# Optimization experiments

Measured on AMD Instinct MI355X. Metric: run time of the kernel, lower is better.

## Reference

```python
import jax, jax.numpy as jnp
import numpy as np

N_HEAD = 16
W = 128  # one-sided window = attention_window // 2


def setup_inputs() -> dict:
    key = jax.random.key(0)
    ks = jax.random.split(key, 6)
    B, S, D = 4, 1536, 1024
    init = lambda k: jax.random.normal(k, (D, D), jnp.float32) * 0.02
    return {
        "x": jax.random.normal(ks[0], (B, S, D), jnp.float32),
        "Wq": init(ks[1]), "bq": jnp.zeros((D,), jnp.float32),
        "Wk": init(ks[2]),
        "Wv": init(ks[3]), "bv": jnp.zeros((D,), jnp.float32),
        "Wo": init(ks[4]), "bo": jnp.zeros((D,), jnp.float32),
    }


def _local_attention(q, k, v, w):
    """Sliding-window attention. q,k,v: [B,H,S,Dh]; q,k pre-scaled.
    Returns context [B,H,S,Dh] and banded logits qk [B,S,H,2w+1] (fp32)."""
    B, H, S, Dh = q.shape
    C = S // w  # number of w-sized query chunks
    pad = [(0, 0), (0, 0), (w, w), (0, 0)]
    kp = jnp.pad(k, pad)
    vp = jnp.pad(v, pad)
    # key/value chunks: chunk c sees padded positions [c*w, c*w + 3w)
    idx = jnp.arange(C)[:, None] * w + jnp.arange(3 * w)[None, :]  # [C,3w]
    kc = kp[:, :, idx]                      # [B,H,C,3w,Dh]
    vc = vp[:, :, idx]                      # [B,H,C,3w,Dh]
    qc = q.reshape(B, H, C, w, Dh)          # [B,H,C,w,Dh]
    scores = jnp.einsum('bhcxd,bhcyd->bhcxy', qc, kc)  # [B,H,C,w,3w]
    # extract diagonal band: query x attends to chunk-local keys y = x .. x+2w
    xi = jnp.arange(w)[:, None]             # [w,1]
    jj = jnp.arange(2 * w + 1)[None, :]     # [1,2w+1]
    y = xi + jj                             # [w,2w+1], values in [0,3w)
    band = jnp.take_along_axis(scores, y[None, None, None], axis=-1)  # [B,H,C,w,2w+1]
    # mask positions whose absolute key index falls outside [0,S)
    key_pos = jnp.arange(C)[:, None, None] * w + xi[None] + jj[None] - w  # [C,w,2w+1]
    valid = (key_pos >= 0) & (key_pos < S)
    band = jnp.where(valid[None, None], band, -jnp.inf)
    prob = jax.nn.softmax(band.astype(jnp.float32), axis=-1).astype(q.dtype)
    # scatter band probs back to chunk layout, then contract with value chunks
    scat = jnp.zeros_like(scores).at[..., xi, y].set(prob)  # [B,H,C,w,3w]
    ctx = jnp.einsum('bhcxy,bhcyd->bhcxd', scat, vc).reshape(B, H, S, Dh)
    qk = band.astype(jnp.float32).reshape(B, H, S, 2 * w + 1).transpose(0, 2, 1, 3)
    return ctx, qk


def reference(x, Wq, bq, Wk, Wv, bv, Wo, bo):
    B, S, D = x.shape
    H, Dh = N_HEAD, D // N_HEAD
    scale = Dh ** (-0.25)
    q = ((x @ Wq.T + bq).reshape(B, S, H, Dh).transpose(0, 2, 1, 3)) * scale
    k = ((x @ Wk.T).reshape(B, S, H, Dh).transpose(0, 2, 1, 3)) * scale
    v = (x @ Wv.T + bv).reshape(B, S, H, Dh).transpose(0, 2, 1, 3)
    ctx, qk = _local_attention(q, k, v, W)
    wv = ctx.transpose(0, 2, 1, 3).reshape(B, S, D)
    out = wv @ Wo.T + bo
    return out, qk
```

## Files before the change

### kernel.cpp

```cpp
#include <hip/hip_runtime.h>

#define S_LEN  1536
#define NH     16
#define DHEAD  64
#define WIN    128
#define BAND   257
#define DMODEL 1024
#define BATCH  4
#define MROWS  (BATCH * S_LEN)

#define SQ    32
#define SWIN  (SQ + 2*WIN)
#define WKEYS 320
#define PST   296

#define NEG_BIG (-3.0e38f)

typedef __attribute__((ext_vector_type(8))) short frag_ab;
typedef __attribute__((ext_vector_type(4))) float frag_cd;
typedef __attribute__((ext_vector_type(8))) unsigned short ushort8v;

__device__ __forceinline__ unsigned short f2bf(float f) {
  unsigned u = __float_as_uint(f);
  u += 0x7FFFu + ((u >> 16) & 1u);
  return (unsigned short)(u >> 16);
}
__device__ __forceinline__ float bf2f(unsigned short h) {
  return __uint_as_float(((unsigned)h) << 16);
}

__device__ __forceinline__ void gload16(const unsigned short* g, unsigned short* l) {
  __builtin_amdgcn_global_load_lds(
      (const __attribute__((address_space(1))) unsigned int*)g,
      (__attribute__((address_space(3))) unsigned int*)l, 16, 0, 0);
}

__global__ __launch_bounds__(256)
void convert_hilo(const float* __restrict__ src, unsigned short* __restrict__ hi,
                  unsigned short* __restrict__ lo, int n4)
{
  const int i = blockIdx.x * 256 + threadIdx.x;
  if (i >= n4) return;
  const float4 v = reinterpret_cast<const float4*>(src)[i];
  unsigned short h0 = f2bf(v.x), h1 = f2bf(v.y), h2 = f2bf(v.z), h3 = f2bf(v.w);
  unsigned short l0 = f2bf(v.x - bf2f(h0)), l1 = f2bf(v.y - bf2f(h1));
  unsigned short l2 = f2bf(v.z - bf2f(h2)), l3 = f2bf(v.w - bf2f(h3));
  uint2 hp, lp;
  hp.x = (unsigned)h0 | ((unsigned)h1 << 16); hp.y = (unsigned)h2 | ((unsigned)h3 << 16);
  lp.x = (unsigned)l0 | ((unsigned)l1 << 16); lp.y = (unsigned)l2 | ((unsigned)l3 << 16);
  reinterpret_cast<uint2*>(hi)[i] = hp;
  reinterpret_cast<uint2*>(lo)[i] = lp;
}

__global__ __launch_bounds__(256)
void copy_f4(const float4* __restrict__ src, float4* __restrict__ dst, int n4)
{
  const int i = blockIdx.x * 256 + threadIdx.x;
  if (i < n4) dst[i] = src[i];
}

__global__ __launch_bounds__(256)
void mfma_gemm_bt(const unsigned short* __restrict__ Ah_g,
                  const unsigned short* __restrict__ Al_g,
                  const unsigned short* __restrict__ Bh_g,
                  const unsigned short* __restrict__ Bl_g,
                  const float* __restrict__ bias, float scale,
                  float* __restrict__ Cf,
                  unsigned short* __restrict__ Ch,
                  unsigned short* __restrict__ Cl, int mode)
{
  __shared__ __align__(16) unsigned short Ah[128*32];
  __shared__ __align__(16) unsigned short Al[128*32];
  __shared__ __align__(16) unsigned short Bh[64*32];
  __shared__ __align__(16) unsigned short Bl[64*32];

  const int t    = threadIdx.x;
  const int wave = t >> 6, lane = t & 63;
  const int wr   = wave >> 1, wc = wave & 1;
  const int m0   = blockIdx.y * 128;
  const int n0   = blockIdx.x * 64;

  frag_cd acc[4][2];
#pragma unroll
  for (int i = 0; i < 4; ++i)
#pragma unroll
    for (int j = 0; j < 2; ++j) acc[i][j] = (frag_cd){0.f,0.f,0.f,0.f};

  const int srow = lane >> 2;
  const int scol = (lane & 3) * 8;
  const unsigned short* pa0 = Ah_g + (size_t)(m0 + wave*32      + srow) * DMODEL + scol;
  const unsigned short* pa1 = Ah_g + (size_t)(m0 + wave*32 + 16 + srow) * DMODEL + scol;
  const unsigned short* qa0 = Al_g + (size_t)(m0 + wave*32      + srow) * DMODEL + scol;
  const unsigned short* qa1 = Al_g + (size_t)(m0 + wave*32 + 16 + srow) * DMODEL + scol;
  const unsigned short* pb  = Bh_g + (size_t)(n0 + wave*16      + srow) * DMODEL + scol;
  const unsigned short* qb  = Bl_g + (size_t)(n0 + wave*16      + srow) * DMODEL + scol;
  unsigned short* lA0 = &Ah[(wave*32)*32];
  unsigned short* lA1 = &Ah[(wave*32+16)*32];
  unsigned short* lL0 = &Al[(wave*32)*32];
  unsigned short* lL1 = &Al[(wave*32+16)*32];
  unsigned short* lB  = &Bh[(wave*16)*32];
  unsigned short* lBl = &Bl[(wave*16)*32];

  const int l16  = lane & 15;
  const int koff = (lane >> 4) * 8;
  int ofsA[4], ofsB[2];
#pragma unroll
  for (int i = 0; i < 4; ++i) ofsA[i] = (wr*64 + i*16 + l16)*32 + koff;
#pragma unroll
  for (int j = 0; j < 2; ++j) ofsB[j] = (wc*32 + j*16 + l16)*32 + koff;

  for (int k0 = 0; k0 < DMODEL; k0 += 32) {
    gload16(pa0, lA0); gload16(pa1, lA1);
    gload16(qa0, lL0); gload16(qa1, lL1);
    gload16(pb,  lB);  gload16(qb,  lBl);
    pa0 += 32; pa1 += 32; qa0 += 32; qa1 += 32; pb += 32; qb += 32;
    __syncthreads();

    frag_ab ah[4], alr[4], bh[2], blr[2];
#pragma unroll
    for (int i = 0; i < 4; ++i) {
      ah[i]  = *reinterpret_cast<const frag_ab*>(&Ah[ofsA[i]]);
      alr[i] = *reinterpret_cast<const frag_ab*>(&Al[ofsA[i]]);
    }
#pragma unroll
    for (int j = 0; j < 2; ++j) {
      bh[j]  = *reinterpret_cast<const frag_ab*>(&Bh[ofsB[j]]);
      blr[j] = *reinterpret_cast<const frag_ab*>(&Bl[ofsB[j]]);
    }
#pragma unroll
    for (int i = 0; i < 4; ++i)
#pragma unroll
      for (int j = 0; j < 2; ++j) {
        acc[i][j] = __builtin_amdgcn_mfma_f32_16x16x32_bf16(ah[i],  bh[j],  acc[i][j], 0,0,0);
        acc[i][j] = __builtin_amdgcn_mfma_f32_16x16x32_bf16(ah[i],  blr[j], acc[i][j], 0,0,0);
        acc[i][j] = __builtin_amdgcn_mfma_f32_16x16x32_bf16(alr[i], bh[j],  acc[i][j], 0,0,0);
      }
    __syncthreads();
  }

  const int rg = lane >> 4;
#pragma unroll
  for (int j = 0; j < 2; ++j) {
    const int n = n0 + wc*32 + j*16 + l16;
    const float bval = bias ? bias[n] : 0.f;
#pragma unroll
    for (int i = 0; i < 4; ++i) {
#pragma unroll
      for (int r = 0; r < 4; ++r) {
        const int m = m0 + wr*64 + i*16 + rg*4 + r;
        const float v = (acc[i][j][r] + bval) * scale;
        if (mode) {
          const int b = m / S_LEN;
          const int s = m - b * S_LEN;
          const int hh = n >> 6, dh = n & 63;
          const size_t idx = ((size_t)((b*NH + hh)*S_LEN + s))*DHEAD + dh;
          const unsigned short hv = f2bf(v);
          Ch[idx] = hv;
          Cl[idx] = f2bf(v - bf2f(hv));
        } else {
          Cf[(size_t)m * DMODEL + n] = v;
        }
      }
    }
  }
}

__global__ __launch_bounds__(256, 3)
void attn_fused(const unsigned short* __restrict__ Qh_g, const unsigned short* __restrict__ Ql_g,
                const unsigned short* __restrict__ Kh_g, const unsigned short* __restrict__ Kl_g,
                const unsigned short* __restrict__ Vh_g, const unsigned short* __restrict__ Vl_g,
                float* __restrict__ qk,
                unsigned short* __restrict__ ctx_hi, unsigned short* __restrict__ ctx_lo)
{
  __shared__ __align__(16) unsigned char arena[48384];
  unsigned short* Khs = (unsigned short*)(arena);
  unsigned short* Kls = (unsigned short*)(arena + 20480);
  unsigned short* Qhs = (unsigned short*)(arena + 40960);
  unsigned short* Qls = (unsigned short*)(arena + 43008);
  unsigned short* Pth = (unsigned short*)(arena);
  unsigned short* Ptl = (unsigned short*)(arena + 18944);
  float*          red = (float*)(arena + 37888);
  unsigned short* Vs  = (unsigned short*)(arena + 38912);

  const int t    = threadIdx.x;
  const int wave = t >> 6, lane = t & 63;

  const int lid  = blockIdx.x;
  const int xcd  = lid & 7;
  const int idx  = lid >> 3;
  const int qblk = xcd*6 + (idx % 6);
  const int hb   = idx / 6;
  const int h    = hb & 15, b = hb >> 4;
  const int qa0  = qblk * SQ;
  const int ws0  = qa0 - WIN;

  const size_t ho = (size_t)(b*NH + h) * S_LEN * DHEAD;
  const unsigned short* Qh = Qh_g + ho;
  const unsigned short* Ql = Ql_g + ho;
  const unsigned short* Kh = Kh_g + ho;
  const unsigned short* Kl = Kl_g + ho;
  const unsigned short* Vh = Vh_g + ho;
  const unsigned short* Vl = Vl_g + ho;

  const int l16  = lane & 15;
  const int grp  = lane >> 4;
  const int koff = grp * 8;
  const int srow = lane >> 2;
  const int scol = (lane & 3) * 8;

  frag_cd acc[2][5];
#pragma unroll
  for (int tm = 0; tm < 2; ++tm)
#pragma unroll
    for (int tn = 0; tn < 5; ++tn) acc[tm][tn] = (frag_cd){0.f,0.f,0.f,0.f};

  for (int p = 0; p < 2; ++p) {
    const int d0 = p * 32;
    if (p) __syncthreads();
#pragma unroll
    for (int i = 0; i < 5; ++i) {
      const int r0 = wave*80 + i*16;
      const ptrdiff_t g = (ptrdiff_t)(ws0 + r0 + srow) * DHEAD + d0 + scol;
      gload16(Kh + g, &Khs[r0*32]);
      gload16(Kl + g, &Kls[r0*32]);
    }
    if (wave < 2) {
      const unsigned short* src = wave ? Ql : Qh;
      unsigned short* dst = wave ? Qls : Qhs;
#pragma unroll
      for (int i = 0; i < 2; ++i) {
        const ptrdiff_t g = (ptrdiff_t)(qa0 + i*16 + srow) * DHEAD + d0 + scol;
        gload16(src + g, &dst[i*16*32]);
      }
    }
    __syncthreads();

    frag_ab ah[2], al[2];
#pragma unroll
    for (int tm = 0; tm < 2; ++tm) {
      const int o = (tm*16 + l16)*32 + koff;
      ah[tm] = *reinterpret_cast<const frag_ab*>(&Qhs[o]);
      al[tm] = *reinterpret_cast<const frag_ab*>(&Qls[o]);
    }
#pragma unroll
    for (int tn = 0; tn < 5; ++tn) {
      const int o = (wave*80 + tn*16 + l16)*32 + koff;
      frag_ab bh = *reinterpret_cast<const frag_ab*>(&Khs[o]);
      frag_ab bl = *reinterpret_cast<const frag_ab*>(&Kls[o]);
#pragma unroll
      for (int tm = 0; tm < 2; ++tm) {
        acc[tm][tn] = __builtin_amdgcn_mfma_f32_16x16x32_bf16(ah[tm], bh, acc[tm][tn], 0,0,0);
        acc[tm][tn] = __builtin_amdgcn_mfma_f32_16x16x32_bf16(ah[tm], bl, acc[tm][tn], 0,0,0);
        acc[tm][tn] = __builtin_amdgcn_mfma_f32_16x16x32_bf16(al[tm], bh, acc[tm][tn], 0,0,0);
      }
    }
  }

#pragma unroll
  for (int tm = 0; tm < 2; ++tm)
#pragma unroll
    for (int tn = 0; tn < 5; ++tn)
#pragma unroll
      for (int r = 0; r < 4; ++r) {
        const int x  = tm*16 + grp*4 + r;
        const int yw = wave*80 + tn*16 + l16;
        const int j  = yw - x;
        const int kp = ws0 + yw;
        const bool ok = (j >= 0) & (j < BAND) & (kp >= 0) & (kp < S_LEN);
        acc[tm][tn][r] = ok ? acc[tm][tn][r] : NEG_BIG;
      }
#pragma unroll
  for (int tm = 0; tm < 2; ++tm)
#pragma unroll
    for (int r = 0; r < 4; ++r) {
      const int x = tm*16 + grp*4 + r;
      float* qrow = qk + ((size_t)(b*S_LEN + qa0 + x)*NH + h) * BAND;
#pragma unroll
      for (int tn = 0; tn < 5; ++tn) {
        const int yw = wave*80 + tn*16 + l16;
        const int j  = yw - x;
        if (j >= 0 && j < BAND) qrow[j] = acc[tm][tn][r];
      }
    }

  __syncthreads();

  const unsigned short* vsrc = (wave == 3) ? Vl : Vh;
  const int vrow0 = (wave == 3) ? 8 : 0;
  ushort8v RA[5], RB[5];

  auto loadVto = [&](int c, ushort8v* R) {
    const int d0 = c*8;
#pragma unroll
    for (int it = 0; it < 5; ++it) {
      const int y = it*64 + lane;
      ushort8v v = {0,0,0,0,0,0,0,0};
      if (y < SWIN) {
        const int kp = ws0 + y;
        if (kp >= 0 && kp < S_LEN)
          v = *reinterpret_cast<const ushort8v*>(vsrc + (size_t)kp*DHEAD + d0);
      }
      R[it] = v;
    }
  };
  auto writeVfrom = [&](ushort8v* R) {
#pragma unroll
    for (int it = 0; it < 5; ++it) {
      const int y = it*64 + lane;
      if (y < SWIN) {
#pragma unroll
        for (int e = 0; e < 8; ++e) Vs[(vrow0 + e)*PST + y] = R[it][e];
      }
    }
  };

  if (wave >= 2) loadVto(0, RA);
#pragma unroll
  for (int tm = 0; tm < 2; ++tm)
#pragma unroll
    for (int r = 0; r < 4; ++r) {
      float m = acc[tm][0][r];
#pragma unroll
      for (int tn = 1; tn < 5; ++tn) m = fmaxf(m, acc[tm][tn][r]);
      m = fmaxf(m, __shfl_xor(m, 1, 64));
      m = fmaxf(m, __shfl_xor(m, 2, 64));
      m = fmaxf(m, __shfl_xor(m, 4, 64));
      m = fmaxf(m, __shfl_xor(m, 8, 64));
      if (l16 == 0) red[(0*4 + wave)*32 + tm*16 + grp*4 + r] = m;
    }
  {
    const uint4 z = make_uint4(0u,0u,0u,0u);
    uint4* pz = reinterpret_cast<uint4*>(arena);
    for (int i = t; i < 37888/16; i += 256) pz[i] = z;
  }
  if (wave >= 2) writeVfrom(RA);
  __syncthreads();

  if (wave >= 2) loadVto(1, RA);
#pragma unroll
  for (int tm = 0; tm < 2; ++tm)
#pragma unroll
    for (int r = 0; r < 4; ++r) {
      const int x = tm*16 + grp*4 + r;
      float m = red[0*128 + 0*32 + x];
      m = fmaxf(m, red[0*128 + 1*32 + x]);
      m = fmaxf(m, red[0*128 + 2*32 + x]);
      m = fmaxf(m, red[0*128 + 3*32 + x]);
      float s = 0.f;
#pragma unroll
      for (int tn = 0; tn < 5; ++tn) {
        const float e = __expf(acc[tm][tn][r] - m);
        acc[tm][tn][r] = e;
        s += e;
      }
      s += __shfl_xor(s, 1, 64);
      s += __shfl_xor(s, 2, 64);
      s += __shfl_xor(s, 4, 64);
      s += __shfl_xor(s, 8, 64);
      if (l16 == 0) red[(1*4 + wave)*32 + x] = s;
    }
  __syncthreads();

#pragma unroll
  for (int tm = 0; tm < 2; ++tm)
#pragma unroll
    for (int r = 0; r < 4; ++r) {
      const int x = tm*16 + grp*4 + r;
      const float gs = red[128 + 0*32 + x] + red[128 + 1*32 + x]
                     + red[128 + 2*32 + x] + red[128 + 3*32 + x];
      const float inv = 1.f / gs;
#pragma unroll
      for (int tn = 0; tn < 5; ++tn) {
        const int yw = wave*80 + tn*16 + l16;
        const int j  = yw - x;
        if (yw < SWIN && j >= 0 && j < BAND) {
          const float p = acc[tm][tn][r] * inv;
          const unsigned short ph = f2bf(p);
          Pth[x*PST + yw] = ph;
          Ptl[x*PST + yw] = f2bf(p - bf2f(ph));
        }
      }
    }
  __syncthreads();

  frag_ab phf[9];
  if (wave < 2) {
#pragma unroll
    for (int ks = 0; ks < 9; ++ks)
      phf[ks] = *reinterpret_cast<const frag_ab*>(&Pth[(wave*16 + l16)*PST + ks*32 + koff]);
  }

#pragma unroll
  for (int c = 0; c < 8; ++c) {
    frag_cd pacc = (frag_cd){0.f,0.f,0.f,0.f};
    if (wave < 2) {
#pragma unroll
      for (int ks = 0; ks < 9; ++ks) {
        const int kk = ks*32 + koff;
        frag_ab pl = *reinterpret_cast<const frag_ab*>(&Ptl[(wave*16 + l16)*PST + kk]);
        frag_ab vb = *reinterpret_cast<const frag_ab*>(&Vs[l16*PST + kk]);
        pacc = __builtin_amdgcn_mfma_f32_16x16x32_bf16(phf[ks], vb, pacc, 0,0,0);
        pacc = __builtin_amdgcn_mfma_f32_16x16x32_bf16(pl,      vb, pacc, 0,0,0);
      }
    } else {
      if (c < 6) loadVto(c + 2, (c & 1) ? RA : RB);
    }
    __syncthreads();
    if (wave < 2) {
#pragma unroll
      for (int r = 0; r < 4; ++r) pacc[r] += __shfl_xor(pacc[r], 8, 64);
      if (l16 < 8) {
        const int d = c*8 + l16;
#pragma unroll
        for (int r = 0; r < 4; ++r) {
          const int x = wave*16 + grp*4 + r;
          const size_t oidx = ((size_t)(b*S_LEN + qa0 + x))*DMODEL + h*DHEAD + d;
          const float v = pacc[r];
          const unsigned short hv = f2bf(v);
          ctx_hi[oidx] = hv;
          ctx_lo[oidx] = f2bf(v - bf2f(hv));
        }
      }
    } else {
      if (c < 7) writeVfrom((c & 1) ? RB : RA);
    }
    if (c < 7) __syncthreads();
  }
}

extern "C" void kernel_launch(void* const* d_in, const int* in_sizes, int n_in,
                              void* d_out, int out_size, void* d_ws, size_t ws_size,
                              hipStream_t stream) {
  const float* x  = (const float*)d_in[0];
  const float* Wq = (const float*)d_in[1];
  const float* bq = (const float*)d_in[2];
  const float* Wk = (const float*)d_in[3];
  const float* Wv = (const float*)d_in[4];
  const float* bv = (const float*)d_in[5];
  const float* Wo = (const float*)d_in[6];
  const float* bo = (const float*)d_in[7];

  float* out = (float*)d_out;
  float* qk  = out + (size_t)MROWS * DMODEL;

  const size_t NX = (size_t)MROWS * DMODEL;
  const size_t NW = (size_t)DMODEL * DMODEL;

  unsigned short* xh  = (unsigned short*)qk;
  unsigned short* xl  = xh  + NX;
  unsigned short* wqh = xl  + NX;
  unsigned short* wql = wqh + NW;
  unsigned short* wkh = wql + NW;
  unsigned short* wkl = wkh + NW;
  unsigned short* wvh = wkl + NW;
  unsigned short* wvl = wvh + NW;

  unsigned short* Qh = (unsigned short*)d_ws;
  unsigned short* Ql = Qh + NX;
  unsigned short* Kh = Ql + NX;
  unsigned short* Kl = Kh + NX;
  unsigned short* Vh = Kl + NX;
  unsigned short* Vl = Vh + NX;

  unsigned short* ctxh = (unsigned short*)out;
  unsigned short* ctxl = ctxh + NX;
  unsigned short* woh  = Kh;
  unsigned short* wol  = Kh + NW;
  float* outTmp = (float*)d_ws;

  const float scale = 0.35355339059327373f;

  dim3 blk(256);
  hipLaunchKernelGGL(convert_hilo, dim3(NX/1024), blk, 0, stream, x,  xh,  xl,  (int)(NX/4));
  hipLaunchKernelGGL(convert_hilo, dim3(NW/1024), blk, 0, stream, Wq, wqh, wql, (int)(NW/4));
  hipLaunchKernelGGL(convert_hilo, dim3(NW/1024), blk, 0, stream, Wk, wkh, wkl, (int)(NW/4));
  hipLaunchKernelGGL(convert_hilo, dim3(NW/1024), blk, 0, stream, Wv, wvh, wvl, (int)(NW/4));

  dim3 gg(DMODEL/64, MROWS/128);
  hipLaunchKernelGGL(mfma_gemm_bt, gg, blk, 0, stream, xh, xl, wqh, wql, bq,      scale,
                     (float*)nullptr, Qh, Ql, 1);
  hipLaunchKernelGGL(mfma_gemm_bt, gg, blk, 0, stream, xh, xl, wkh, wkl, nullptr, scale,
                     (float*)nullptr, Kh, Kl, 1);
  hipLaunchKernelGGL(mfma_gemm_bt, gg, blk, 0, stream, xh, xl, wvh, wvl, bv,      1.0f,
                     (float*)nullptr, Vh, Vl, 1);

  hipLaunchKernelGGL(attn_fused, dim3((S_LEN/SQ)*NH*BATCH), blk, 0, stream,
                     Qh, Ql, Kh, Kl, Vh, Vl, qk, ctxh, ctxl);

  hipLaunchKernelGGL(convert_hilo, dim3(NW/1024), blk, 0, stream, Wo, woh, wol, (int)(NW/4));

  hipLaunchKernelGGL(mfma_gemm_bt, gg, blk, 0, stream, ctxh, ctxl, woh, wol, bo, 1.0f,
                     outTmp, (unsigned short*)nullptr, (unsigned short*)nullptr, 0);
  hipLaunchKernelGGL(copy_f4, dim3(NX/1024), blk, 0, stream,
                     (const float4*)outTmp, (float4*)out, (int)(NX/4));
}
```

Baseline: 492.2 us.

## Fuse Q/K/V projections into one 128x128-tile GEMM with XCD-aware block mapping

```diff
diff --git a/kernel.cpp b/kernel.cpp
--- a/kernel.cpp
+++ b/kernel.cpp
@@ -60,14 +60,129 @@
 }
 
 __global__ __launch_bounds__(256)
+void mfma_gemm_qkv(const unsigned short* __restrict__ Ah_g,
+                   const unsigned short* __restrict__ Al_g,
+                   const unsigned short* __restrict__ Bh_g,
+                   const unsigned short* __restrict__ Bl_g,
+                   const float* __restrict__ bq, const float* __restrict__ bv,
+                   float scale,
+                   unsigned short* __restrict__ Qh, unsigned short* __restrict__ Ql,
+                   unsigned short* __restrict__ Kh, unsigned short* __restrict__ Kl,
+                   unsigned short* __restrict__ Vh, unsigned short* __restrict__ Vl)
+{
+  __shared__ __align__(16) unsigned short Ah[128*32];
+  __shared__ __align__(16) unsigned short Al[128*32];
+  __shared__ __align__(16) unsigned short Bh[128*32];
+  __shared__ __align__(16) unsigned short Bl[128*32];
+
+  const int t    = threadIdx.x;
+  const int wave = t >> 6, lane = t & 63;
+  const int wr   = wave >> 1, wc = wave & 1;
+
+  const int bid  = blockIdx.x;
+  const int xcd  = bid & 7;
+  const int r    = bid >> 3;
+  const int n0   = (xcd*3 + (r % 3)) * 128;
+  const int m0   = (r / 3) * 128;
+
+  frag_cd acc[4][4];
+#pragma unroll
+  for (int i = 0; i < 4; ++i)
+#pragma unroll
+    for (int j = 0; j < 4; ++j) acc[i][j] = (frag_cd){0.f,0.f,0.f,0.f};
+
+  const int srow = lane >> 2;
+  const int scol = (lane & 3) * 8;
+  const unsigned short* pa0 = Ah_g + (size_t)(m0 + wave*32      + srow) * DMODEL + scol;
+  const unsigned short* pa1 = Ah_g + (size_t)(m0 + wave*32 + 16 + srow) * DMODEL + scol;
+  const unsigned short* qa0 = Al_g + (size_t)(m0 + wave*32      + srow) * DMODEL + scol;
+  const unsigned short* qa1 = Al_g + (size_t)(m0 + wave*32 + 16 + srow) * DMODEL + scol;
+  const unsigned short* pb0 = Bh_g + (size_t)(n0 + wave*32      + srow) * DMODEL + scol;
+  const unsigned short* pb1 = Bh_g + (size_t)(n0 + wave*32 + 16 + srow) * DMODEL + scol;
+  const unsigned short* qb0 = Bl_g + (size_t)(n0 + wave*32      + srow) * DMODEL + scol;
+  const unsigned short* qb1 = Bl_g + (size_t)(n0 + wave*32 + 16 + srow) * DMODEL + scol;
+  unsigned short* lA0 = &Ah[(wave*32)*32];
+  unsigned short* lA1 = &Ah[(wave*32+16)*32];
+  unsigned short* lL0 = &Al[(wave*32)*32];
+  unsigned short* lL1 = &Al[(wave*32+16)*32];
+  unsigned short* lB0 = &Bh[(wave*32)*32];
+  unsigned short* lB1 = &Bh[(wave*32+16)*32];
+  unsigned short* lC0 = &Bl[(wave*32)*32];
+  unsigned short* lC1 = &Bl[(wave*32+16)*32];
+
+  const int l16  = lane & 15;
+  const int koff = (lane >> 4) * 8;
+  int ofsA[4], ofsB[4];
+#pragma unroll
+  for (int i = 0; i < 4; ++i) ofsA[i] = (wr*64 + i*16 + l16)*32 + koff;
+#pragma unroll
+  for (int j = 0; j < 4; ++j) ofsB[j] = (wc*64 + j*16 + l16)*32 + koff;
+
+  for (int k0 = 0; k0 < DMODEL; k0 += 32) {
+    gload16(pa0, lA0); gload16(pa1, lA1);
+    gload16(qa0, lL0); gload16(qa1, lL1);
+    gload16(pb0, lB0); gload16(pb1, lB1);
+    gload16(qb0, lC0); gload16(qb1, lC1);
+    pa0 += 32; pa1 += 32; qa0 += 32; qa1 += 32;
+    pb0 += 32; pb1 += 32; qb0 += 32; qb1 += 32;
+    __syncthreads();
+
+    frag_ab ah[4], alr[4];
+#pragma unroll
+    for (int i = 0; i < 4; ++i) {
+      ah[i]  = *reinterpret_cast<const frag_ab*>(&Ah[ofsA[i]]);
+      alr[i] = *reinterpret_cast<const frag_ab*>(&Al[ofsA[i]]);
+    }
+#pragma unroll
+    for (int j = 0; j < 4; ++j) {
+      frag_ab bh  = *reinterpret_cast<const frag_ab*>(&Bh[ofsB[j]]);
+      frag_ab blr = *reinterpret_cast<const frag_ab*>(&Bl[ofsB[j]]);
+#pragma unroll
+      for (int i = 0; i < 4; ++i) {
+        acc[i][j] = __builtin_amdgcn_mfma_f32_16x16x32_bf16(ah[i],  bh,  acc[i][j], 0,0,0);
+        acc[i][j] = __builtin_amdgcn_mfma_f32_16x16x32_bf16(ah[i],  blr, acc[i][j], 0,0,0);
+        acc[i][j] = __builtin_amdgcn_mfma_f32_16x16x32_bf16(alr[i], bh,  acc[i][j], 0,0,0);
+      }
+    }
+    __syncthreads();
+  }
+
+  const int rg = lane >> 4;
+  const int which = n0 >> 10;
+  const float sc = (which < 2) ? scale : 1.0f;
+  const float* bias = (which == 0) ? bq : ((which == 2) ? bv : nullptr);
+  unsigned short* Dh = (which == 0) ? Qh : ((which == 1) ? Kh : Vh);
+  unsigned short* Dl = (which == 0) ? Ql : ((which == 1) ? Kl : Vl);
+#pragma unroll
+  for (int j = 0; j < 4; ++j) {
+    const int n  = n0 + wc*64 + j*16 + l16;
+    const int nn = n & 1023;
+    const float bval = bias ? bias[nn] : 0.f;
+    const int hh = nn >> 6, dh = nn & 63;
+#pragma unroll
+    for (int i = 0; i < 4; ++i) {
+#pragma unroll
+      for (int r2 = 0; r2 < 4; ++r2) {
+        const int m = m0 + wr*64 + i*16 + rg*4 + r2;
+        const int b = m / S_LEN;
+        const int s = m - b * S_LEN;
+        const size_t idx = ((size_t)((b*NH + hh)*S_LEN + s))*DHEAD + dh;
+        const float v = (acc[i][j][r2] + bval) * sc;
+        const unsigned short hv = f2bf(v);
+        Dh[idx] = hv;
+        Dl[idx] = f2bf(v - bf2f(hv));
+      }
+    }
+  }
+}
+
+__global__ __launch_bounds__(256)
 void mfma_gemm_bt(const unsigned short* __restrict__ Ah_g,
                   const unsigned short* __restrict__ Al_g,
                   const unsigned short* __restrict__ Bh_g,
                   const unsigned short* __restrict__ Bl_g,
                   const float* __restrict__ bias, float scale,
-                  float* __restrict__ Cf,
-                  unsigned short* __restrict__ Ch,
-                  unsigned short* __restrict__ Cl, int mode)
+                  float* __restrict__ Cf)
 {
   __shared__ __align__(16) unsigned short Ah[128*32];
   __shared__ __align__(16) unsigned short Al[128*32];
@@ -148,18 +263,7 @@
 #pragma unroll
       for (int r = 0; r < 4; ++r) {
         const int m = m0 + wr*64 + i*16 + rg*4 + r;
-        const float v = (acc[i][j][r] + bval) * scale;
-        if (mode) {
-          const int b = m / S_LEN;
-          const int s = m - b * S_LEN;
-          const int hh = n >> 6, dh = n & 63;
-          const size_t idx = ((size_t)((b*NH + hh)*S_LEN + s))*DHEAD + dh;
-          const unsigned short hv = f2bf(v);
-          Ch[idx] = hv;
-          Cl[idx] = f2bf(v - bf2f(hv));
-        } else {
-          Cf[(size_t)m * DMODEL + n] = v;
-        }
+        Cf[(size_t)m * DMODEL + n] = (acc[i][j][r] + bval) * scale;
       }
     }
   }
@@ -448,12 +552,8 @@
 
   unsigned short* xh  = (unsigned short*)qk;
   unsigned short* xl  = xh  + NX;
-  unsigned short* wqh = xl  + NX;
-  unsigned short* wql = wqh + NW;
-  unsigned short* wkh = wql + NW;
-  unsigned short* wkl = wkh + NW;
-  unsigned short* wvh = wkl + NW;
-  unsigned short* wvl = wvh + NW;
+  unsigned short* whc = xl  + NX;
+  unsigned short* wlc = whc + 3*NW;
 
   unsigned short* Qh = (unsigned short*)d_ws;
   unsigned short* Ql = Qh + NX;
@@ -472,25 +572,22 @@
 
   dim3 blk(256);
   hipLaunchKernelGGL(convert_hilo, dim3(NX/1024), blk, 0, stream, x,  xh,  xl,  (int)(NX/4));
-  hipLaunchKernelGGL(convert_hilo, dim3(NW/1024), blk, 0, stream, Wq, wqh, wql, (int)(NW/4));
-  hipLaunchKernelGGL(convert_hilo, dim3(NW/1024), blk, 0, stream, Wk, wkh, wkl, (int)(NW/4));
-  hipLaunchKernelGGL(convert_hilo, dim3(NW/1024), blk, 0, stream, Wv, wvh, wvl, (int)(NW/4));
-
-  dim3 gg(DMODEL/64, MROWS/128);
-  hipLaunchKernelGGL(mfma_gemm_bt, gg, blk, 0, stream, xh, xl, wqh, wql, bq,      scale,
-                     (float*)nullptr, Qh, Ql, 1);
-  hipLaunchKernelGGL(mfma_gemm_bt, gg, blk, 0, stream, xh, xl, wkh, wkl, nullptr, scale,
-                     (float*)nullptr, Kh, Kl, 1);
-  hipLaunchKernelGGL(mfma_gemm_bt, gg, blk, 0, stream, xh, xl, wvh, wvl, bv,      1.0f,
-                     (float*)nullptr, Vh, Vl, 1);
+  hipLaunchKernelGGL(convert_hilo, dim3(NW/1024), blk, 0, stream, Wq, whc,        wlc,        (int)(NW/4));
+  hipLaunchKernelGGL(convert_hilo, dim3(NW/1024), blk, 0, stream, Wk, whc + NW,   wlc + NW,   (int)(NW/4));
+  hipLaunchKernelGGL(convert_hilo, dim3(NW/1024), blk, 0, stream, Wv, whc + 2*NW, wlc + 2*NW, (int)(NW/4));
+
+  hipLaunchKernelGGL(mfma_gemm_qkv, dim3(1152), blk, 0, stream,
+                     xh, xl, whc, wlc, bq, bv, scale,
+                     Qh, Ql, Kh, Kl, Vh, Vl);
 
   hipLaunchKernelGGL(attn_fused, dim3((S_LEN/SQ)*NH*BATCH), blk, 0, stream,
                      Qh, Ql, Kh, Kl, Vh, Vl, qk, ctxh, ctxl);
 
   hipLaunchKernelGGL(convert_hilo, dim3(NW/1024), blk, 0, stream, Wo, woh, wol, (int)(NW/4));
 
+  dim3 gg(DMODEL/64, MROWS/128);
   hipLaunchKernelGGL(mfma_gemm_bt, gg, blk, 0, stream, ctxh, ctxl, woh, wol, bo, 1.0f,
-                     outTmp, (unsigned short*)nullptr, (unsigned short*)nullptr, 0);
+                     outTmp);
   hipLaunchKernelGGL(copy_f4, dim3(NX/1024), blk, 0, stream,
                      (const float4*)outTmp, (float4*)out, (int)(NX/4));
 }
```

Result: faster. 481.9 us (-2.1%).
